# Kernel tuning notes

Measured on AMD Instinct MI355X. Metric: run time of the kernel, lower is better.

The kernel has to match this reference:

```python
import jax, jax.numpy as jnp
import numpy as np

NUM_HEADS = 8
D_MODEL = 512
HEAD_DIM = D_MODEL // NUM_HEADS
LN_EPS = 1e-5


def setup_inputs() -> dict:
    key = jax.random.key(0)
    ks = jax.random.split(key, 12)
    B, S = 8, 1024
    P = 2 * S - 1  # relative position length
    s = 0.02
    return {
        "x": jax.random.normal(ks[0], (B, S, D_MODEL), jnp.float32),
        "pos_emb": jax.random.normal(ks[1], (P, D_MODEL), jnp.float32),
        "ln_w": jnp.ones((D_MODEL,), jnp.float32),
        "ln_b": jnp.zeros((D_MODEL,), jnp.float32),
        "Wq": jax.random.normal(ks[2], (D_MODEL, D_MODEL), jnp.float32) * s,
        "bq": jax.random.normal(ks[3], (D_MODEL,), jnp.float32) * s,
        "Wk": jax.random.normal(ks[4], (D_MODEL, D_MODEL), jnp.float32) * s,
        "bk": jax.random.normal(ks[5], (D_MODEL,), jnp.float32) * s,
        "Wv": jax.random.normal(ks[6], (D_MODEL, D_MODEL), jnp.float32) * s,
        "bv": jax.random.normal(ks[7], (D_MODEL,), jnp.float32) * s,
        "Wo": jax.random.normal(ks[8], (D_MODEL, D_MODEL), jnp.float32) * s,
        "bo": jax.random.normal(ks[9], (D_MODEL,), jnp.float32) * s,
        "Wp": jax.random.normal(ks[10], (D_MODEL, D_MODEL), jnp.float32) * s,
        "pos_bias_u": jax.random.normal(ks[11], (D_MODEL,), jnp.float32) * s,
        "pos_bias_v": jax.random.normal(jax.random.fold_in(key, 99), (D_MODEL,), jnp.float32) * s,
    }


def _rel_shift(x):
    # x: [B, H, S, P] -> Transformer-XL relative shift, return [B, H, S, S]
    b, h, s, p = x.shape
    x = jnp.pad(x, ((0, 0), (0, 0), (0, 0), (1, 0)))  # pad one zero column on left
    x = x.reshape(b, h, p + 1, s)[:, :, 1:, :]
    x = x.reshape(b, h, s, p)
    return x[:, :, :, :s]


def reference(x, pos_emb, ln_w, ln_b, Wq, bq, Wk, bk, Wv, bv, Wo, bo, Wp,
              pos_bias_u, pos_bias_v):
    B, S, D = x.shape
    H, hd = NUM_HEADS, HEAD_DIM
    # LayerNorm
    mu = jnp.mean(x, axis=-1, keepdims=True)
    var = jnp.mean(jnp.square(x - mu), axis=-1, keepdims=True)
    h_ = (x - mu) * jax.lax.rsqrt(var + LN_EPS) * ln_w + ln_b
    # Projections (torch Linear: y = x @ W.T + b)
    q = (h_ @ Wq.T + bq).reshape(B, S, H, hd).transpose(0, 2, 1, 3)  # [B,H,S,hd]
    k = (h_ @ Wk.T + bk).reshape(B, S, H, hd).transpose(0, 2, 1, 3)
    v = (h_ @ Wv.T + bv).reshape(B, S, H, hd).transpose(0, 2, 1, 3)
    bias_u = pos_bias_u.reshape(1, H, 1, hd)
    bias_v = pos_bias_v.reshape(1, H, 1, hd)
    content = jnp.einsum('bhqd,bhkd->bhqk', q + bias_u, k)
    # Positional projection: [P, D] -> [H, P, hd]
    p = (pos_emb @ Wp.T).reshape(-1, H, hd).transpose(1, 0, 2)
    pos_score = jnp.einsum('bhqd,hpd->bhqp', q + bias_v, p)
    pos_score = _rel_shift(pos_score)
    scale = 1.0 / np.sqrt(hd).astype(np.float32)
    attn = jax.nn.softmax((content + pos_score) * scale, axis=-1)
    out = jnp.einsum('bhqk,bhkd->bhqd', attn, v)
    out = out.transpose(0, 2, 1, 3).reshape(B, S, D)
    out = out @ Wo.T + bo
    return x + out
```

## Files before the change

kernel.cpp:

```cpp
#include <hip/hip_runtime.h>
#include <hip/hip_bf16.h>


typedef __attribute__((ext_vector_type(8))) short  s16x8;
typedef __attribute__((ext_vector_type(8))) __bf16 bfv8;
typedef __attribute__((ext_vector_type(4))) float  f32x4;
typedef __attribute__((ext_vector_type(4))) unsigned u32x4;

__device__ __forceinline__ float b2f(short s){
  unsigned u = ((unsigned)(unsigned short)s) << 16;
  float f; __builtin_memcpy(&f, &u, 4); return f;
}
__device__ __forceinline__ short f2b(float f){
  unsigned u; __builtin_memcpy(&u, &f, 4);
  u = (u + 0x7fffu + ((u >> 16) & 1u)) >> 16;
  return (short)u;
}
__device__ __forceinline__ unsigned pk2(float lo, float hi){
  __hip_bfloat162 t = __float22bfloat162_rn(make_float2(lo, hi));
  unsigned u; __builtin_memcpy(&u, &t, 4); return u;
}
__device__ __forceinline__ f32x4 MFMA(s16x8 a, s16x8 b, f32x4 c){
  return __builtin_amdgcn_mfma_f32_16x16x32_bf16(
      __builtin_bit_cast(bfv8, a), __builtin_bit_cast(bfv8, b), c, 0, 0, 0);
}
__device__ __forceinline__ void gload_lds16(const void* g, void* l){
  __builtin_amdgcn_global_load_lds(
      (const __attribute__((address_space(1))) void*)g,
      (__attribute__((address_space(3))) void*)l, 16, 0, 0);
}
__device__ __forceinline__ void cvt8(const float* in, short* out, size_t i8){
  f32x4 a = *(const f32x4*)(in + i8*8);
  f32x4 b = *(const f32x4*)(in + i8*8 + 4);
  u32x4 o;
  o[0] = pk2(a[0],a[1]); o[1] = pk2(a[2],a[3]);
  o[2] = pk2(b[0],b[1]); o[3] = pk2(b[2],b[3]);
  *(u32x4*)(out + i8*8) = o;
}

__global__ __launch_bounds__(256) void prep_kernel(
    const float* __restrict__ Wq, const float* __restrict__ Wk,
    const float* __restrict__ Wv, const float* __restrict__ Wo,
    const float* __restrict__ Wp, const float* __restrict__ pos,
    const float* __restrict__ x, const float* __restrict__ lnw, const float* __restrict__ lnb,
    short* __restrict__ wqkv, short* __restrict__ wo, short* __restrict__ wp,
    short* __restrict__ posbf, short* __restrict__ h_bf)
{
  int bid = blockIdx.x, tid = threadIdx.x;
  if(bid < 640){
    int w = bid >> 7;
    size_t i = (size_t)(bid & 127)*256 + tid;
    const float* src; short* dst;
    if(w == 0){ src = Wq; dst = wqkv; }
    else if(w == 1){ src = Wk; dst = wqkv + 262144; }
    else if(w == 2){ src = Wv; dst = wqkv + 524288; }
    else if(w == 3){ src = Wo; dst = wo; }
    else { src = Wp; dst = wp; }
    cvt8(src, dst, i);
  } else if(bid < 1152){
    size_t i = (size_t)(bid - 640)*256 + tid;
    if(i < 131008) cvt8(pos, posbf, i);
  } else {
    int row = (bid - 1152)*4 + (tid >> 6);
    int lane = tid & 63;
    const float* xr = x + (size_t)row*512;
    f32x4 v0 = *(const f32x4*)(xr + lane*8);
    f32x4 v1 = *(const f32x4*)(xr + lane*8 + 4);
    float s  = v0[0]+v0[1]+v0[2]+v0[3]+v1[0]+v1[1]+v1[2]+v1[3];
    float s2 = v0[0]*v0[0]+v0[1]*v0[1]+v0[2]*v0[2]+v0[3]*v0[3]
             + v1[0]*v1[0]+v1[1]*v1[1]+v1[2]*v1[2]+v1[3]*v1[3];
    #pragma unroll
    for(int m=1;m<64;m<<=1){ s += __shfl_xor(s,m); s2 += __shfl_xor(s2,m); }
    float mu = s * (1.0f/512.0f);
    float rs = rsqrtf(s2*(1.0f/512.0f) - mu*mu + 1e-5f);
    float y[8];
    #pragma unroll
    for(int e=0;e<8;e++){
      float xv = (e<4)? v0[e] : v1[e-4];
      int d = lane*8 + e;
      y[e] = (xv - mu)*rs*lnw[d] + lnb[d];
    }
    u32x4 o;
    o[0]=pk2(y[0],y[1]); o[1]=pk2(y[2],y[3]); o[2]=pk2(y[4],y[5]); o[3]=pk2(y[6],y[7]);
    *(u32x4*)(h_bf + (size_t)row*512 + lane*8) = o;
  }
}

__global__ __launch_bounds__(256) void gemm_fused(
    const short* __restrict__ h_bf, const short* __restrict__ wqkv,
    const float* __restrict__ bq, const float* __restrict__ bk, const float* __restrict__ bv,
    const short* __restrict__ posbf, const short* __restrict__ wp,
    short* __restrict__ q_sw, short* __restrict__ k_sw, short* __restrict__ v_sw,
    short* __restrict__ p_sw)
{
  __shared__ __align__(16) short smem[16384];
  short* At = smem;
  short* Bt = smem + 8192;
  int bid = blockIdx.x, tid = threadIdx.x;
  int wave = tid >> 6, lane = tid & 63;
  int quad = lane >> 4, l16 = lane & 15;
  int srow8 = lane >> 3, scol8 = (lane & 7)*8;
  if(bid < 768){
    int bx = bid % 12, by = bid / 12;
    int m0 = by*128, n0 = bx*128;
    int wm = wave >> 1, wn = wave & 1;
    f32x4 acc[4][4] = {};
    for(int k0=0; k0<512; k0+=64){
      #pragma unroll
      for(int c=0;c<4;c++){
        int u = wave*4 + c;
        gload_lds16(h_bf + (size_t)(m0 + u*8 + srow8)*512 + k0 + scol8, At + u*512);
        gload_lds16(wqkv + (size_t)(n0 + u*8 + srow8)*512 + k0 + scol8, Bt + u*512);
      }
      __syncthreads();
      #pragma unroll
      for(int ks=0; ks<2; ks++){
        s16x8 af[4], bfr[4];
        #pragma unroll
        for(int i=0;i<4;i++) af[i]  = *(const s16x8*)(At + (wm*64 + i*16 + l16)*64 + ks*32 + quad*8);
        #pragma unroll
        for(int j=0;j<4;j++) bfr[j] = *(const s16x8*)(Bt + (wn*64 + j*16 + l16)*64 + ks*32 + quad*8);
        #pragma unroll
        for(int i=0;i<4;i++)
          #pragma unroll
          for(int j=0;j<4;j++)
            acc[i][j] = MFMA(af[i], bfr[j], acc[i][j]);
      }
      __syncthreads();
    }
    int seg = bx >> 2;
    int nseg = (bx & 3)*128;
    int bb = by >> 3;
    const float* bsrc = (seg==0)? bq : (seg==1)? bk : bv;
    float bias_j[4];
    #pragma unroll
    for(int j=0;j<4;j++) bias_j[j] = bsrc[nseg + wn*64 + j*16 + l16];
    if(seg < 2){
      short* dst = seg ? k_sw : q_sw;
      #pragma unroll
      for(int h2=0; h2<2; h2++){
        if(wm == h2){
          #pragma unroll
          for(int i=0;i<4;i++){
            int lr = i*16 + quad*4;
            #pragma unroll
            for(int j=0;j<4;j++){
              int cl = wn*64 + j*16 + l16;
              unsigned p01 = pk2(acc[i][j][0]+bias_j[j], acc[i][j][1]+bias_j[j]);
              unsigned p23 = pk2(acc[i][j][2]+bias_j[j], acc[i][j][3]+bias_j[j]);
              smem[(lr+0)*136 + cl] = (short)p01;
              smem[(lr+1)*136 + cl] = (short)(p01>>16);
              smem[(lr+2)*136 + cl] = (short)p23;
              smem[(lr+3)*136 + cl] = (short)(p23>>16);
            }
          }
        }
        __syncthreads();
        #pragma unroll
        for(int it=0; it<4; it++){
          int ci = it*4 + wave;
          int hs = ci >> 2, tb = ci & 3;
          s16x8 vv = *(const s16x8*)(smem + (tb*16 + l16)*136 + hs*32 + quad*8);
          int hh = (nseg>>6) + (hs>>1);
          int tg = ((m0 + h2*64)>>4) + tb;
          size_t chunk = ((size_t)((bb*8 + hh)*64 + tg))*2 + (hs&1);
          *(s16x8*)(dst + chunk*512 + (size_t)lane*8) = vv;
        }
        __syncthreads();
      }
    } else {
      #pragma unroll
      for(int h2=0; h2<2; h2++){
        int jt = by*2 + h2;
        if(wm == h2){
          #pragma unroll
          for(int i=0;i<4;i++){
            int tl = i*16 + quad*4;
            #pragma unroll
            for(int j=0;j<4;j++){
              int dl = wn*64 + j*16 + l16;
              unsigned p01 = pk2(acc[i][j][0]+bias_j[j], acc[i][j][1]+bias_j[j]);
              unsigned p23 = pk2(acc[i][j][2]+bias_j[j], acc[i][j][3]+bias_j[j]);
              unsigned* w2 = (unsigned*)(smem + dl*72 + tl);
              w2[0] = p01; w2[1] = p23;
            }
          }
        }
        __syncthreads();
        #pragma unroll
        for(int it=0; it<4; it++){
          int ci = it*4 + wave;
          int hl = ci>>3, ds = (ci>>1)&3, jk = ci&1;
          s16x8 vv = *(const s16x8*)(smem + (hl*64 + ds*16 + l16)*72 + jk*32 + quad*8);
          int hh = (nseg>>6) + hl;
          size_t chunk = (((size_t)((bb*8 + hh)*16 + jt))*4 + ds)*2 + jk;
          *(s16x8*)(v_sw + chunk*512 + (size_t)lane*8) = vv;
        }
        __syncthreads();
      }
    }
  } else {
    int pid = bid - 768;
    int bx = pid % 8, by = pid / 8;
    int m0 = by*64, n0 = bx*64;
    int wm = wave >> 1, wn = wave & 1;
    f32x4 acc[2][2] = {};
    for(int k0=0; k0<512; k0+=64){
      #pragma unroll
      for(int c=0;c<2;c++){
        int u = wave*2 + c;
        int ra = m0 + u*8 + srow8; if(ra > 2046) ra = 2046;
        gload_lds16(posbf + (size_t)ra*512 + k0 + scol8, At + u*512);
        gload_lds16(wp + (size_t)(n0 + u*8 + srow8)*512 + k0 + scol8, Bt + u*512);
      }
      __syncthreads();
      #pragma unroll
      for(int ks=0; ks<2; ks++){
        s16x8 af[2], bfr[2];
        #pragma unroll
        for(int i=0;i<2;i++) af[i]  = *(const s16x8*)(At + (wm*32 + i*16 + l16)*64 + ks*32 + quad*8);
        #pragma unroll
        for(int j=0;j<2;j++) bfr[j] = *(const s16x8*)(Bt + (wn*32 + j*16 + l16)*64 + ks*32 + quad*8);
        #pragma unroll
        for(int i=0;i<2;i++)
          #pragma unroll
          for(int j=0;j<2;j++)
            acc[i][j] = MFMA(af[i], bfr[j], acc[i][j]);
      }
      __syncthreads();
    }
    #pragma unroll
    for(int i=0;i<2;i++){
      int rowb = m0 + wm*32 + i*16 + quad*4;
      #pragma unroll
      for(int j=0;j<2;j++){
        int col = n0 + wn*32 + j*16 + l16;
        int hh = col>>6, ks = (col>>5)&1, qd = (col>>3)&3, e = col&7;
        int rblk = rowb>>4;
        size_t base = ((size_t)(((hh*128+rblk)*2+ks)*64) + qd*16)*8 + e;
        #pragma unroll
        for(int r=0;r<4;r++)
          p_sw[base + (size_t)(quad*4+r)*8] = f2b(acc[i][j][r]);
      }
    }
  }
}

__global__ __launch_bounds__(512, 1) void attn_kernel(
    const short* __restrict__ q_sw, const short* __restrict__ k_sw,
    const short* __restrict__ v_sw, const short* __restrict__ p_sw,
    const float* __restrict__ bu, const float* __restrict__ bvv,
    short* __restrict__ out)
{
  __shared__ __align__(16) short kv[2][8192];
  __shared__ __align__(16) short pwall[16384];
  int tid = threadIdx.x;
  int wave = tid >> 6, lane = tid & 63, quad = lane >> 4, l16 = lane & 15;
  int h = blockIdx.y, b = blockIdx.z, bh = b*8 + h;
  int qt = blockIdx.x;
  int iblk32 = qt*8 + wave;
  int iw = iblk32*32;
  short* pw = pwall + wave*2048;

  const short* qb = q_sw + (size_t)bh*65536;
  const short* kb = k_sw + (size_t)bh*65536;
  const short* vb = v_sw + (size_t)bh*65536;
  const short* pb = p_sw + (size_t)h*131072;

  s16x8 qu[2][2], qv[2][2];
  #pragma unroll
  for(int s=0;s<2;s++){
    #pragma unroll
    for(int ks=0;ks<2;ks++){
      s16x8 qr = *(const s16x8*)(qb + ((size_t)((iblk32*2+s)*2+ks)*64 + lane)*8);
      short tu[8], tv[8];
      #pragma unroll
      for(int e=0;e<8;e++){
        int d = h*64 + ks*32 + quad*8 + e;
        float f = b2f(qr[e]);
        tu[e] = f2b((f + bu[d]) * 0.125f);
        tv[e] = f2b((f + bvv[d]) * 0.125f);
      }
      qu[s][ks] = *(s16x8*)tu; qv[s][ks] = *(s16x8*)tv;
    }
  }

  s16x8 ones;
  #pragma unroll
  for(int e=0;e<8;e++) ones[e] = (short)0x3F80;

  int srcl[4]; bool lo[4];
  #pragma unroll
  for(int r=0;r<4;r++){
    int il = quad*4 + r;
    srcl[r] = quad*16 + ((l16 + 15 - il) & 15);
    lo[r]   = (l16 <= il);
  }

  f32x4 oacc[2][4] = {};
  f32x4 lacc[2] = {};
  s16x8 Pa[6][2];

  auto STAGE = [&](int jt, int bufi){
    const short* base = (wave < 4) ? kb : vb;
    #pragma unroll
    for(int r=0;r<2;r++){
      int unit = wave*2 + r;
      gload_lds16(base + (size_t)jt*4096 + (unit&7)*512 + lane*8,
                  &kv[bufi][unit*512]);
    }
  };
  auto LOADPOS = [&](int jt){
    int rb0 = (jt*64 - iw + 1008) >> 4;
    #pragma unroll
    for(int nt=0;nt<6;nt++)
      #pragma unroll
      for(int ks=0;ks<2;ks++)
        Pa[nt][ks] = *(const s16x8*)(pb + (size_t)((rb0-1+nt)*2+ks)*512 + lane*8);
  };
  auto COMPUTE = [&](const short* Kt, const short* Vt, int next_jt){
    f32x4 ps0[5], ps1[5];
    __builtin_amdgcn_s_setprio(1);
    #pragma unroll
    for(int nt=0;nt<6;nt++){
      s16x8 pf0 = Pa[nt][0], pf1 = Pa[nt][1];
      if(nt >= 1){
        f32x4 a = {};
        a = MFMA(qv[0][0], pf0, a);
        a = MFMA(qv[0][1], pf1, a);
        ps0[nt-1] = a;
      }
      if(nt <= 4){
        f32x4 a = {};
        a = MFMA(qv[1][0], pf0, a);
        a = MFMA(qv[1][1], pf1, a);
        ps1[nt] = a;
      }
    }
    __builtin_amdgcn_s_setprio(0);
    if(next_jt < 16) LOADPOS(next_jt);
    float rot0[4][5], rot1[4][5];
    #pragma unroll
    for(int r=0;r<4;r++){
      #pragma unroll
      for(int nt=0;nt<5;nt++){
        rot0[r][nt] = __shfl(ps0[nt][r], srcl[r]);
        rot1[r][nt] = __shfl(ps1[nt][r], srcl[r]);
      }
    }
    #pragma unroll
    for(int js=0;js<4;js++){
      s16x8 kf0 = *(const s16x8*)(Kt + (js*2+0)*512 + lane*8);
      s16x8 kf1 = *(const s16x8*)(Kt + (js*2+1)*512 + lane*8);
      int col = js*16 + l16;
      int r0 = quad*4;
      {
        f32x4 c0;
        #pragma unroll
        for(int r=0;r<4;r++) c0[r] = lo[r] ? rot0[r][js] : rot0[r][js+1];
        f32x4 a = MFMA(qu[0][0], kf0, c0);
        a = MFMA(qu[0][1], kf1, a);
        unsigned p01 = pk2(__expf(a[0]), __expf(a[1]));
        unsigned p23 = pk2(__expf(a[2]), __expf(a[3]));
        pw[((r0+0)*64 + col) ^ (((r0+0)&7)<<3)] = (short)p01;
        pw[((r0+1)*64 + col) ^ (((r0+1)&7)<<3)] = (short)(p01>>16);
        pw[((r0+2)*64 + col) ^ (((r0+2)&7)<<3)] = (short)p23;
        pw[((r0+3)*64 + col) ^ (((r0+3)&7)<<3)] = (short)(p23>>16);
      }
      {
        f32x4 c0;
        #pragma unroll
        for(int r=0;r<4;r++) c0[r] = lo[r] ? rot1[r][js] : rot1[r][js+1];
        f32x4 a = MFMA(qu[1][0], kf0, c0);
        a = MFMA(qu[1][1], kf1, a);
        unsigned p01 = pk2(__expf(a[0]), __expf(a[1]));
        unsigned p23 = pk2(__expf(a[2]), __expf(a[3]));
        pw[1024 + (((r0+0)*64 + col) ^ (((r0+0)&7)<<3))] = (short)p01;
        pw[1024 + (((r0+1)*64 + col) ^ (((r0+1)&7)<<3))] = (short)(p01>>16);
        pw[1024 + (((r0+2)*64 + col) ^ (((r0+2)&7)<<3))] = (short)p23;
        pw[1024 + (((r0+3)*64 + col) ^ (((r0+3)&7)<<3))] = (short)(p23>>16);
      }
    }
    __builtin_amdgcn_s_setprio(1);
    #pragma unroll
    for(int jk=0;jk<2;jk++){
      int po = (l16*64 + jk*32 + quad*8) ^ ((l16&7)<<3);
      s16x8 pa0 = *(const s16x8*)(pw + po);
      s16x8 pa1 = *(const s16x8*)(pw + 1024 + po);
      lacc[0] = MFMA(pa0, ones, lacc[0]);
      lacc[1] = MFMA(pa1, ones, lacc[1]);
      #pragma unroll
      for(int ds=0;ds<4;ds++){
        s16x8 vf = *(const s16x8*)(Vt + (ds*2+jk)*512 + lane*8);
        oacc[0][ds] = MFMA(pa0, vf, oacc[0][ds]);
        oacc[1][ds] = MFMA(pa1, vf, oacc[1][ds]);
      }
    }
    __builtin_amdgcn_s_setprio(0);
  };

  STAGE(0, 0);
  LOADPOS(0);
  __syncthreads();

  #pragma unroll 1
  for(int jt2=0; jt2<8; ++jt2){
    int jt = jt2*2;
    STAGE(jt+1, 1);
    COMPUTE(&kv[0][0], &kv[0][4096], jt+1);
    __syncthreads();
    if(jt2 < 7) STAGE(jt+2, 0);
    COMPUTE(&kv[1][0], &kv[1][4096], jt+2);
    __syncthreads();
  }

  #pragma unroll
  for(int s=0;s<2;s++){
    float rl[4];
    #pragma unroll
    for(int r=0;r<4;r++) rl[r] = __builtin_amdgcn_rcpf(lacc[s][r]);
    #pragma unroll
    for(int ds=0; ds<4; ds++)
      #pragma unroll
      for(int r=0;r<4;r++)
        out[((size_t)(b*1024 + iw + s*16 + quad*4 + r))*512 + h*64 + ds*16 + l16] =
            f2b(oacc[s][ds][r] * rl[r]);
  }
}

__global__ __launch_bounds__(256) void gemm_out(
    const short* __restrict__ A, const short* __restrict__ B,
    const float* __restrict__ bias, const float* __restrict__ resid,
    float* __restrict__ Cout)
{
  __shared__ __align__(16) short At[128*64];
  __shared__ __align__(16) short Bt[128*64];
  int tid = threadIdx.x;
  int wave = tid >> 6, lane = tid & 63;
  int quad = lane >> 4, l16 = lane & 15;
  int wm = wave >> 1, wn = wave & 1;
  int m0 = blockIdx.y*128, n0 = blockIdx.x*128;
  int srow8 = lane >> 3, scol8 = (lane & 7)*8;
  f32x4 acc[4][4] = {};
  for(int k0=0; k0<512; k0+=64){
    #pragma unroll
    for(int c=0;c<4;c++){
      int u = wave*4 + c;
      gload_lds16(A + (size_t)(m0 + u*8 + srow8)*512 + k0 + scol8, At + u*512);
      gload_lds16(B + (size_t)(n0 + u*8 + srow8)*512 + k0 + scol8, Bt + u*512);
    }
    __syncthreads();
    #pragma unroll
    for(int ks=0; ks<2; ks++){
      s16x8 af[4], bfr[4];
      #pragma unroll
      for(int i=0;i<4;i++) af[i]  = *(const s16x8*)(At + (wm*64 + i*16 + l16)*64 + ks*32 + quad*8);
      #pragma unroll
      for(int j=0;j<4;j++) bfr[j] = *(const s16x8*)(Bt + (wn*64 + j*16 + l16)*64 + ks*32 + quad*8);
      #pragma unroll
      for(int i=0;i<4;i++)
        #pragma unroll
        for(int j=0;j<4;j++)
          acc[i][j] = MFMA(af[i], bfr[j], acc[i][j]);
    }
    __syncthreads();
  }
  #pragma unroll
  for(int i=0;i<4;i++){
    int rowb = m0 + wm*64 + i*16 + quad*4;
    #pragma unroll
    for(int j=0;j<4;j++){
      int col = n0 + wn*64 + j*16 + l16;
      float bv = bias[col];
      #pragma unroll
      for(int r=0;r<4;r++){
        size_t idx = (size_t)(rowb + r)*512 + col;
        Cout[idx] = acc[i][j][r] + bv + resid[idx];
      }
    }
  }
}

extern "C" void kernel_launch(void* const* d_in, const int* in_sizes, int n_in,
                              void* d_out, int out_size, void* d_ws, size_t ws_size,
                              hipStream_t stream)
{
  const float* x    = (const float*)d_in[0];
  const float* pos  = (const float*)d_in[1];
  const float* lnw  = (const float*)d_in[2];
  const float* lnb  = (const float*)d_in[3];
  const float* Wq   = (const float*)d_in[4];
  const float* bq   = (const float*)d_in[5];
  const float* Wk   = (const float*)d_in[6];
  const float* bk   = (const float*)d_in[7];
  const float* Wv   = (const float*)d_in[8];
  const float* bv   = (const float*)d_in[9];
  const float* Wo   = (const float*)d_in[10];
  const float* bo   = (const float*)d_in[11];
  const float* Wp   = (const float*)d_in[12];
  const float* pbu  = (const float*)d_in[13];
  const float* pbv  = (const float*)d_in[14];
  float* out = (float*)d_out;

  char* ws = (char*)d_ws;
  short* h_bf    = (short*)(ws);
  short* q_sw    = (short*)(ws + ( 8u<<20));
  short* k_sw    = (short*)(ws + (16u<<20));
  short* v_sw    = (short*)(ws + (24u<<20));
  short* a_bf    = (short*)(ws + (32u<<20));
  short* p_sw    = (short*)(ws + (40u<<20));
  short* pos_bf  = (short*)(ws + (42u<<20));
  short* wqkv_bf = (short*)(ws + (44u<<20));
  short* wo_bf   = (short*)(ws + (47u<<20));
  short* wp_bf   = (short*)(ws + (47u<<20) + (512u<<10));

  prep_kernel<<<dim3(3200), 256, 0, stream>>>(Wq, Wk, Wv, Wo, Wp, pos,
                                              x, lnw, lnb,
                                              wqkv_bf, wo_bf, wp_bf, pos_bf, h_bf);
  gemm_fused<<<dim3(1024), 256, 0, stream>>>(h_bf, wqkv_bf, bq, bk, bv,
                                             pos_bf, wp_bf,
                                             q_sw, k_sw, v_sw, p_sw);
  attn_kernel<<<dim3(4,8,8), 512, 0, stream>>>(q_sw, k_sw, v_sw, p_sw, pbu, pbv, a_bf);
  gemm_out<<<dim3(4,64), 256, 0, stream>>>(a_bf, wo_bf, bo, x, out);
  (void)in_sizes; (void)n_in; (void)out_size; (void)ws_size;
}
```

Before: 192.8 us.

## Shrink attention blocks, pad P scratch, stage output epilogue via LDS, vectorize LN params

The attention kernel moves from 512-thread blocks at one block per CU to 256-thread blocks with launch bounds allowing two per CU. The grid doubles and each wave now stages four K/V units instead of two. The per-wave probability scratch drops the XOR swizzle for a padded 72-element row stride to avoid bank conflicts. The output GEMM epilogue writes accumulators plus bias into LDS, then does coalesced float4 residual adds and stores, at the cost of extra syncs. LayerNorm weight and bias are loaded as float4 vectors.

```diff
diff --git a/kernel.cpp b/kernel.cpp
--- a/kernel.cpp
+++ b/kernel.cpp
@@ -66,6 +66,10 @@
     const float* xr = x + (size_t)row*512;
     f32x4 v0 = *(const f32x4*)(xr + lane*8);
     f32x4 v1 = *(const f32x4*)(xr + lane*8 + 4);
+    f32x4 w0 = *(const f32x4*)(lnw + lane*8);
+    f32x4 w1 = *(const f32x4*)(lnw + lane*8 + 4);
+    f32x4 c0 = *(const f32x4*)(lnb + lane*8);
+    f32x4 c1 = *(const f32x4*)(lnb + lane*8 + 4);
     float s  = v0[0]+v0[1]+v0[2]+v0[3]+v1[0]+v1[1]+v1[2]+v1[3];
     float s2 = v0[0]*v0[0]+v0[1]*v0[1]+v0[2]*v0[2]+v0[3]*v0[3]
              + v1[0]*v1[0]+v1[1]*v1[1]+v1[2]*v1[2]+v1[3]*v1[3];
@@ -77,8 +81,9 @@
     #pragma unroll
     for(int e=0;e<8;e++){
       float xv = (e<4)? v0[e] : v1[e-4];
-      int d = lane*8 + e;
-      y[e] = (xv - mu)*rs*lnw[d] + lnb[d];
+      float wv = (e<4)? w0[e] : w1[e-4];
+      float bv = (e<4)? c0[e] : c1[e-4];
+      y[e] = (xv - mu)*rs*wv + bv;
     }
     u32x4 o;
     o[0]=pk2(y[0],y[1]); o[1]=pk2(y[2],y[3]); o[2]=pk2(y[4],y[5]); o[3]=pk2(y[6],y[7]);
@@ -246,21 +251,21 @@
   }
 }
 
-__global__ __launch_bounds__(512, 1) void attn_kernel(
+__global__ __launch_bounds__(256, 2) void attn_kernel(
     const short* __restrict__ q_sw, const short* __restrict__ k_sw,
     const short* __restrict__ v_sw, const short* __restrict__ p_sw,
     const float* __restrict__ bu, const float* __restrict__ bvv,
     short* __restrict__ out)
 {
   __shared__ __align__(16) short kv[2][8192];
-  __shared__ __align__(16) short pwall[16384];
+  __shared__ __align__(16) short pwall[9216];
   int tid = threadIdx.x;
   int wave = tid >> 6, lane = tid & 63, quad = lane >> 4, l16 = lane & 15;
   int h = blockIdx.y, b = blockIdx.z, bh = b*8 + h;
   int qt = blockIdx.x;
-  int iblk32 = qt*8 + wave;
+  int iblk32 = qt*4 + wave;
   int iw = iblk32*32;
-  short* pw = pwall + wave*2048;
+  short* pw = pwall + wave*2304;
 
   const short* qb = q_sw + (size_t)bh*65536;
   const short* kb = k_sw + (size_t)bh*65536;
@@ -302,10 +307,10 @@
   s16x8 Pa[6][2];
 
   auto STAGE = [&](int jt, int bufi){
-    const short* base = (wave < 4) ? kb : vb;
-    #pragma unroll
-    for(int r=0;r<2;r++){
-      int unit = wave*2 + r;
+    const short* base = (wave < 2) ? kb : vb;
+    #pragma unroll
+    for(int r=0;r<4;r++){
+      int unit = wave*4 + r;
       gload_lds16(base + (size_t)jt*4096 + (unit&7)*512 + lane*8,
                   &kv[bufi][unit*512]);
     }
@@ -353,7 +358,6 @@
       s16x8 kf0 = *(const s16x8*)(Kt + (js*2+0)*512 + lane*8);
       s16x8 kf1 = *(const s16x8*)(Kt + (js*2+1)*512 + lane*8);
       int col = js*16 + l16;
-      int r0 = quad*4;
       {
         f32x4 c0;
         #pragma unroll
@@ -362,10 +366,10 @@
         a = MFMA(qu[0][1], kf1, a);
         unsigned p01 = pk2(__expf(a[0]), __expf(a[1]));
         unsigned p23 = pk2(__expf(a[2]), __expf(a[3]));
-        pw[((r0+0)*64 + col) ^ (((r0+0)&7)<<3)] = (short)p01;
-        pw[((r0+1)*64 + col) ^ (((r0+1)&7)<<3)] = (short)(p01>>16);
-        pw[((r0+2)*64 + col) ^ (((r0+2)&7)<<3)] = (short)p23;
-        pw[((r0+3)*64 + col) ^ (((r0+3)&7)<<3)] = (short)(p23>>16);
+        pw[(quad*4+0)*72 + col] = (short)p01;
+        pw[(quad*4+1)*72 + col] = (short)(p01>>16);
+        pw[(quad*4+2)*72 + col] = (short)p23;
+        pw[(quad*4+3)*72 + col] = (short)(p23>>16);
       }
       {
         f32x4 c0;
@@ -375,18 +379,17 @@
         a = MFMA(qu[1][1], kf1, a);
         unsigned p01 = pk2(__expf(a[0]), __expf(a[1]));
         unsigned p23 = pk2(__expf(a[2]), __expf(a[3]));
-        pw[1024 + (((r0+0)*64 + col) ^ (((r0+0)&7)<<3))] = (short)p01;
-        pw[1024 + (((r0+1)*64 + col) ^ (((r0+1)&7)<<3))] = (short)(p01>>16);
-        pw[1024 + (((r0+2)*64 + col) ^ (((r0+2)&7)<<3))] = (short)p23;
-        pw[1024 + (((r0+3)*64 + col) ^ (((r0+3)&7)<<3))] = (short)(p23>>16);
+        pw[1152 + (quad*4+0)*72 + col] = (short)p01;
+        pw[1152 + (quad*4+1)*72 + col] = (short)(p01>>16);
+        pw[1152 + (quad*4+2)*72 + col] = (short)p23;
+        pw[1152 + (quad*4+3)*72 + col] = (short)(p23>>16);
       }
     }
     __builtin_amdgcn_s_setprio(1);
     #pragma unroll
     for(int jk=0;jk<2;jk++){
-      int po = (l16*64 + jk*32 + quad*8) ^ ((l16&7)<<3);
-      s16x8 pa0 = *(const s16x8*)(pw + po);
-      s16x8 pa1 = *(const s16x8*)(pw + 1024 + po);
+      s16x8 pa0 = *(const s16x8*)(pw + l16*72 + jk*32 + quad*8);
+      s16x8 pa1 = *(const s16x8*)(pw + 1152 + l16*72 + jk*32 + quad*8);
       lacc[0] = MFMA(pa0, ones, lacc[0]);
       lacc[1] = MFMA(pa1, ones, lacc[1]);
       #pragma unroll
@@ -433,8 +436,9 @@
     const float* __restrict__ bias, const float* __restrict__ resid,
     float* __restrict__ Cout)
 {
-  __shared__ __align__(16) short At[128*64];
-  __shared__ __align__(16) short Bt[128*64];
+  __shared__ __align__(16) short smem[16896];
+  short* At = smem;
+  short* Bt = smem + 8192;
   int tid = threadIdx.x;
   int wave = tid >> 6, lane = tid & 63;
   int quad = lane >> 4, l16 = lane & 15;
@@ -465,19 +469,39 @@
     }
     __syncthreads();
   }
+  float bias_j[4];
   #pragma unroll
-  for(int i=0;i<4;i++){
-    int rowb = m0 + wm*64 + i*16 + quad*4;
-    #pragma unroll
-    for(int j=0;j<4;j++){
-      int col = n0 + wn*64 + j*16 + l16;
-      float bv = bias[col];
-      #pragma unroll
-      for(int r=0;r<4;r++){
-        size_t idx = (size_t)(rowb + r)*512 + col;
-        Cout[idx] = acc[i][j][r] + bv + resid[idx];
-      }
-    }
+  for(int j=0;j<4;j++) bias_j[j] = bias[n0 + wn*64 + j*16 + l16];
+  float* ct = (float*)smem;
+  #pragma unroll
+  for(int h2=0; h2<2; h2++){
+    if(wm == h2){
+      #pragma unroll
+      for(int i=0;i<4;i++){
+        int lr = i*16 + quad*4;
+        #pragma unroll
+        for(int j=0;j<4;j++){
+          int cl = wn*64 + j*16 + l16;
+          #pragma unroll
+          for(int r=0;r<4;r++)
+            ct[(lr+r)*132 + cl] = acc[i][j][r] + bias_j[j];
+        }
+      }
+    }
+    __syncthreads();
+    #pragma unroll
+    for(int it=0; it<8; it++){
+      int idx = it*256 + tid;
+      int row = idx >> 5, c4 = (idx & 31)*4;
+      f32x4 v = *(const f32x4*)(ct + row*132 + c4);
+      size_t gi = (size_t)(m0 + h2*64 + row)*512 + n0 + c4;
+      f32x4 rv = *(const f32x4*)(resid + gi);
+      f32x4 o;
+      #pragma unroll
+      for(int e=0;e<4;e++) o[e] = v[e] + rv[e];
+      *(f32x4*)(Cout + gi) = o;
+    }
+    __syncthreads();
   }
 }
 
@@ -520,7 +544,7 @@
   gemm_fused<<<dim3(1024), 256, 0, stream>>>(h_bf, wqkv_bf, bq, bk, bv,
                                              pos_bf, wp_bf,
                                              q_sw, k_sw, v_sw, p_sw);
-  attn_kernel<<<dim3(4,8,8), 512, 0, stream>>>(q_sw, k_sw, v_sw, p_sw, pbu, pbv, a_bf);
+  attn_kernel<<<dim3(8,8,8), 256, 0, stream>>>(q_sw, k_sw, v_sw, p_sw, pbu, pbv, a_bf);
   gemm_out<<<dim3(4,64), 256, 0, stream>>>(a_bf, wo_bf, bo, x, out);
   (void)in_sizes; (void)n_in; (void)out_size; (void)ws_size;
 }
```

Result: no change. 193.8 us (+0.5%).
